# Optimization experiments

Hardware: AMD Instinct MI355X
Metric: run time of the kernel (lower is better)

The kernel has to match this reference:

```python
import jax, jax.numpy as jnp
import numpy as np

COV_LOSS_WT = 1.0


def setup_inputs() -> dict:
    key = jax.random.key(0)
    ks = jax.random.split(key, 6)
    B, T, S, H = 8, 64, 256, 768
    sc = 1.0 / np.sqrt(H)
    return {
        "decoder_outputs": jax.random.normal(ks[0], (B, T, H), jnp.float32),
        "decoder_input_mask": jnp.ones((B, T), jnp.float32),
        "encoder_outputs": jax.random.normal(ks[1], (B, S, H), jnp.float32),
        "enc_padding_mask": jnp.ones((B, S), jnp.float32),
        "coverage": jnp.zeros((B, S), jnp.float32),
        "W_h": (jax.random.normal(ks[2], (H, H), jnp.float32) * sc),
        "W_dec": (jax.random.normal(ks[3], (H, H), jnp.float32) * sc),
        "b_dec": jnp.zeros((H,), jnp.float32),
        "w_c": (jax.random.normal(ks[4], (H,), jnp.float32) * sc),
        "v": (jax.random.normal(ks[5], (H,), jnp.float32) * sc),
    }


def reference(decoder_outputs, decoder_input_mask, encoder_outputs,
              enc_padding_mask, coverage, W_h, W_dec, b_dec, w_c, v):
    # Precompute projections (same math as expanding att_features then adding
    # the coverage feature per step).
    enc_feature = encoder_outputs @ W_h.T                 # [B,S,H]
    dec_fea = decoder_outputs @ W_dec.T + b_dec           # [B,T,H]

    def step(cov, dec_t):
        # cov: [B,S], dec_t: [B,H]
        e = jnp.tanh(enc_feature + dec_t[:, None, :] + cov[:, :, None] * w_c)  # [B,S,H]
        scores = e @ v                                    # [B,S]
        attn = jax.nn.softmax(scores, axis=-1) * enc_padding_mask
        attn = attn / attn.sum(-1, keepdims=True)
        ht = jnp.einsum('bs,bsh->bh', attn, encoder_outputs)
        step_loss = COV_LOSS_WT * jnp.sum(jnp.minimum(attn, cov), axis=-1)     # [B]
        return cov + attn, (ht, attn, step_loss)

    coverage_final, (ht, attn, step_losses) = jax.lax.scan(
        step, coverage, jnp.swapaxes(dec_fea, 0, 1))      # scan over T

    ht_hat = jnp.swapaxes(ht, 0, 1)                       # [B,T,H]
    attn_dist = jnp.swapaxes(attn, 0, 1)                  # [B,T,S]
    converge_loss = jnp.sum(step_losses * decoder_input_mask.T) / jnp.sum(decoder_input_mask)
    return (ht_hat, attn_dist, converge_loss, coverage_final)
```

## Files before the change

kernel.cpp:

```cpp
#include <hip/hip_runtime.h>

#define Bq 8
#define Tq 64
#define Sq 256
#define Hq 768
#define TT 8
#define ST 8

typedef float f32x4 __attribute__((ext_vector_type(4)));
typedef __bf16 bf16x8 __attribute__((ext_vector_type(8)));

#define TANH_SCALE 2.885390081777927f
#define LOG2E 1.4426950408889634f

template <int Ctrl, int Rmask>
__device__ __forceinline__ float dpp_add_f(float v) {
  int t = __builtin_amdgcn_update_dpp(0, __float_as_int(v), Ctrl, Rmask, 0xF, true);
  return v + __int_as_float(t);
}
__device__ __forceinline__ float wave64_sum(float v) {
  v = dpp_add_f<0xB1, 0xF>(v);
  v = dpp_add_f<0x4E, 0xF>(v);
  v = dpp_add_f<0x141, 0xF>(v);
  v = dpp_add_f<0x140, 0xF>(v);
  v = dpp_add_f<0x142, 0xA>(v);
  v = dpp_add_f<0x143, 0xC>(v);
  return __int_as_float(__builtin_amdgcn_readlane(__float_as_int(v), 63));
}

__device__ __forceinline__ uint2 cvt4(f32x4 v) {
  union { __bf16 h[4]; uint2 u; } t;
  t.h[0] = (__bf16)v[0]; t.h[1] = (__bf16)v[1];
  t.h[2] = (__bf16)v[2]; t.h[3] = (__bf16)v[3];
  return t.u;
}

__global__ __launch_bounds__(256, 4) void proj_kernel(
    const float* __restrict__ enc, const float* __restrict__ dec,
    const float* __restrict__ Wh, const float* __restrict__ Wd,
    const float* __restrict__ bd,
    const float* __restrict__ wcvec, const float* __restrict__ vvec,
    __bf16* __restrict__ efh, __bf16* __restrict__ decfh,
    float* __restrict__ w1g, float* __restrict__ lacc,
    unsigned* __restrict__ cnt)
{
  {
    int gidx = blockIdx.x * 256 + threadIdx.x;
    if (gidx < Hq) w1g[gidx] = vvec[gidx] * wcvec[gidx];
    if (gidx < 64) cnt[gidx] = 0u;
    if (gidx == 0) lacc[0] = 0.f;
  }

  __shared__ unsigned short As[2][32][40];
  __shared__ unsigned short Bs[2][64][40];

  int bid = blockIdx.x;
  const float* A; const float* W; bool isEf;
  int bm, bn;
  if (bid < 768) {
    A = enc; W = Wh; isEf = true;
    bm = bid % 64; bn = bid / 64;
  } else {
    bid -= 768;
    A = dec; W = Wd; isEf = false;
    bm = bid % 16; bn = bid / 16;
  }
  const int m0 = bm * 32, n0 = bn * 64;

  const int ti = threadIdx.x;
  const int rowA = ti >> 3, colA = (ti & 7) * 4;
  const int rowB = ti >> 2, colB = (ti & 3) * 8;
  const float* pa = A + (size_t)(m0 + rowA) * Hq + colA;
  const float* pw = W + (size_t)(n0 + rowB) * Hq + colB;

  {
    f32x4 a0 = *(const f32x4*)pa;
    f32x4 w0 = *(const f32x4*)pw, w1 = *(const f32x4*)(pw + 4);
    *(uint2*)&As[0][rowA][colA]     = cvt4(a0);
    *(uint2*)&Bs[0][rowB][colB]     = cvt4(w0);
    *(uint2*)&Bs[0][rowB][colB + 4] = cvt4(w1);
  }
  __syncthreads();

  const int w = ti >> 6, ln = ti & 63;
  const int mh = (w >> 1) * 16, nh = (w & 1) * 32;
  const int rsel = ln & 15, kofe = (ln >> 4) * 8;

  f32x4 acc[2] = {};
  for (int k = 0; k < 24; k++) {
    f32x4 na, nw0, nw1;
    if (k < 23) {
      na  = *(const f32x4*)(pa + (k + 1) * 32);
      nw0 = *(const f32x4*)(pw + (k + 1) * 32);
      nw1 = *(const f32x4*)(pw + (k + 1) * 32 + 4);
    }
    const int cur = k & 1;
    bf16x8 af = *(const bf16x8*)&As[cur][mh + rsel][kofe];
    bf16x8 b0 = *(const bf16x8*)&Bs[cur][nh + rsel][kofe];
    bf16x8 b1 = *(const bf16x8*)&Bs[cur][nh + 16 + rsel][kofe];
    acc[0] = __builtin_amdgcn_mfma_f32_16x16x32_bf16(af, b0, acc[0], 0, 0, 0);
    acc[1] = __builtin_amdgcn_mfma_f32_16x16x32_bf16(af, b1, acc[1], 0, 0, 0);
    if (k < 23) {
      const int nxt = cur ^ 1;
      *(uint2*)&As[nxt][rowA][colA]     = cvt4(na);
      *(uint2*)&Bs[nxt][rowB][colB]     = cvt4(nw0);
      *(uint2*)&Bs[nxt][rowB][colB + 4] = cvt4(nw1);
      __syncthreads();
    }
  }

  const int col = ln & 15, rb = (ln >> 4) * 4;
#pragma unroll
  for (int tn = 0; tn < 2; tn++)
#pragma unroll
    for (int j = 0; j < 4; j++) {
      int r = m0 + mh + rb + j, c = n0 + nh + tn * 16 + col;
      float val = acc[tn][j];
      if (isEf) {
        efh[(size_t)r * Hq + c] =
            (__bf16)__builtin_amdgcn_exp2f(val * TANH_SCALE);
      } else {
        decfh[(size_t)r * Hq + c] =
            (__bf16)__builtin_amdgcn_exp2f((val + bd[c]) * TANH_SCALE);
      }
    }
}

__global__ __launch_bounds__(256, 6) void abscan_kernel(
    const __bf16* __restrict__ efh, const __bf16* __restrict__ decfh,
    const float* __restrict__ vvec, const float* __restrict__ w1g,
    const float* __restrict__ emask, const float* __restrict__ cov0,
    const float* __restrict__ dmask,
    float2* __restrict__ ab,
    float* __restrict__ out_attn, float* __restrict__ out_covf,
    float* __restrict__ lacc, unsigned* __restrict__ cnt)
{
  __shared__ double smem_raw[3280];
  const int bid = blockIdx.x;
  const int tid = threadIdx.x;

  if (bid < 2048) {
    unsigned short (*efs)[772] = (unsigned short(*)[772])smem_raw;
    unsigned short (*dts)[772] = (unsigned short(*)[772])((char*)smem_raw + 12352);
    float (*part)[64][2]       = (float(*)[64][2])((char*)smem_raw + 24704);
    const int kchunk = bid >> 8;
    const int b = (bid >> 5) & 7;
    const int stile = bid & 31;
    const int tt0 = kchunk * TT;
    const int st0 = stile * ST;

    for (int i = tid; i < ST * 192; i += 256) {
      int row = i / 192, c = (i % 192) * 4;
      *(uint2*)&efs[row][c] =
          *(const uint2*)(efh + (size_t)(b * Sq + st0 + row) * Hq + c);
    }
    for (int i = tid; i < TT * 192; i += 256) {
      int row = i / 192, c = (i % 192) * 4;
      *(uint2*)&dts[row][c] =
          *(const uint2*)(decfh + (size_t)(b * Tq + tt0 + row) * Hq + c);
    }
    __syncthreads();

    const int hh = tid >> 6;
    const int pid = tid & 63;
    const int tl = pid >> 3, sl = pid & 7;
    const int hbase = hh * 192;
    const int hbu = __builtin_amdgcn_readfirstlane(hbase);
    const float* vp  = vvec + hbu;
    const float* w1p = w1g + hbu;

    float A = 0.f, B = 0.f;
#define BLO(x) __uint_as_float((x) << 16)
#define BHI(x) __uint_as_float((x) & 0xFFFF0000u)
#pragma unroll 2
    for (int j = 0; j < 192; j += 8) {
      uint2 eu0 = *(const uint2*)&efs[sl][hbase + j];
      uint2 eu1 = *(const uint2*)&efs[sl][hbase + j + 4];
      uint2 du0 = *(const uint2*)&dts[tl][hbase + j];
      uint2 du1 = *(const uint2*)&dts[tl][hbase + j + 4];
      f32x4 v40 = *(const f32x4*)(vp + j);
      f32x4 v41 = *(const f32x4*)(vp + j + 4);
      f32x4 w10 = *(const f32x4*)(w1p + j);
      f32x4 w11 = *(const f32x4*)(w1p + j + 4);
      float e2[8];
      e2[0] = BLO(eu0.x) * BLO(du0.x);
      e2[1] = BHI(eu0.x) * BHI(du0.x);
      e2[2] = BLO(eu0.y) * BLO(du0.y);
      e2[3] = BHI(eu0.y) * BHI(du0.y);
      e2[4] = BLO(eu1.x) * BLO(du1.x);
      e2[5] = BHI(eu1.x) * BHI(du1.x);
      e2[6] = BLO(eu1.y) * BLO(du1.y);
      e2[7] = BHI(eu1.y) * BHI(du1.y);
#pragma unroll
      for (int e = 0; e < 8; e++) {
        float rr = __builtin_amdgcn_rcpf(1.f + e2[e]);
        float t0 = 1.f - 2.f * rr;
        float f1 = 1.f - t0 * t0;
        float vx = (e < 4) ? v40[e] : v41[e - 4];
        float wx = (e < 4) ? w10[e] : w11[e - 4];
        A += vx * t0;
        B += wx * f1;
      }
    }
#undef BLO
#undef BHI

    if (hh != 0) { part[hh - 1][pid][0] = A; part[hh - 1][pid][1] = B; }
    __syncthreads();
    if (hh == 0) {
      union { float2 f; unsigned long long u; } cv;
      cv.f.x = A + part[0][pid][0] + part[1][pid][0] + part[2][pid][0];
      cv.f.y = B + part[0][pid][1] + part[1][pid][1] + part[2][pid][1];
      __hip_atomic_store(
          (unsigned long long*)&ab[(size_t)(b * Tq + tt0 + tl) * Sq + st0 + sl],
          cv.u, __ATOMIC_RELAXED, __HIP_MEMORY_SCOPE_AGENT);
    }
    __syncthreads();
    if (tid == 0)
      __hip_atomic_fetch_add(&cnt[b * 8 + kchunk], 1u,
                             __ATOMIC_RELAXED, __HIP_MEMORY_SCOPE_AGENT);
  } else {
    if (tid >= 64) return;
    const int b = bid - 2048;
    const int ln = tid;
    float dm = dmask[b * Tq + ln];
    float cov[4], em[4], E[4];
    float lp = 0.f;
#pragma unroll
    for (int i = 0; i < 4; i++) {
      cov[i] = cov0[b * Sq + ln + 64 * i];
      em[i]  = emask[b * Sq + ln + 64 * i];
    }
    const unsigned long long* P =
        (const unsigned long long*)(ab + (size_t)b * Tq * Sq + ln);
    union U64 { unsigned long long u; float2 f; };
    U64 cv0[4], cv1[4];

    for (int kc = 0; kc < 8; kc++) {
      unsigned c;
      do {
        c = __hip_atomic_load(&cnt[b * 8 + kc],
                              __ATOMIC_RELAXED, __HIP_MEMORY_SCOPE_AGENT);
      } while (__builtin_amdgcn_readfirstlane(c) < 32u);

      const int tb = kc * 8;
#pragma unroll
      for (int i = 0; i < 4; i++)
        cv0[i].u = __hip_atomic_load(P + (size_t)tb * Sq + 64 * i,
                                     __ATOMIC_RELAXED, __HIP_MEMORY_SCOPE_AGENT);
#pragma unroll
      for (int i = 0; i < 4; i++)
        cv1[i].u = __hip_atomic_load(P + (size_t)(tb + 1) * Sq + 64 * i,
                                     __ATOMIC_RELAXED, __HIP_MEMORY_SCOPE_AGENT);

#pragma unroll
      for (int j = 0; j < 8; j++) {
        const int t = tb + j;
        float s4 = 0.f;
#pragma unroll
        for (int i = 0; i < 4; i++) {
          float sc = cv0[i].f.x + cov[i] * cv0[i].f.y;
          E[i] = __builtin_amdgcn_exp2f(sc * LOG2E) * em[i];
          s4 += E[i];
        }
#pragma unroll
        for (int i = 0; i < 4; i++) {
          cv0[i] = cv1[i];
          if (j < 6)
            cv1[i].u = __hip_atomic_load(P + (size_t)(t + 2) * Sq + 64 * i,
                                         __ATOMIC_RELAXED, __HIP_MEMORY_SCOPE_AGENT);
        }
        float Z = wave64_sum(s4);
        float invZ = __builtin_amdgcn_rcpf(Z);
        float dmt = __shfl(dm, t);
#pragma unroll
        for (int i = 0; i < 4; i++) {
          float at = E[i] * invZ;
          lp += fminf(at, cov[i]) * dmt;
          cov[i] += at;
          out_attn[(size_t)(b * Tq + t) * Sq + ln + 64 * i] = at;
        }
      }
    }

#pragma unroll
    for (int i = 0; i < 4; i++)
      out_covf[b * Sq + ln + 64 * i] = cov[i];
    float wl = wave64_sum(lp);
    if (ln == 0) atomicAdd(lacc, wl);
  }
}

__global__ __launch_bounds__(256) void ht_kernel(
    const float* __restrict__ attn, const float* __restrict__ enc,
    const float* __restrict__ dmask, const float* __restrict__ lacc,
    float* __restrict__ out_ht, float* __restrict__ out_loss)
{
  __shared__ float lat[Sq][8];
  __shared__ float r4[4];
  int bid = blockIdx.x;
  int b = bid / 24, r = bid % 24, tc = r / 3, hc = r % 3;
  int tid = threadIdx.x;
  int h = hc * 256 + tid;
#pragma unroll
  for (int tt = 0; tt < 8; tt++)
    lat[tid][tt] = attn[(size_t)(b * Tq + tc * 8 + tt) * Sq + tid];
  __syncthreads();

  float acc[8] = {};
  const float* ep = enc + (size_t)(b * Sq) * Hq + h;
  for (int sb = 0; sb < Sq; sb += 8) {
    float e[8];
#pragma unroll
    for (int u = 0; u < 8; u++) e[u] = ep[(size_t)(sb + u) * Hq];
#pragma unroll
    for (int u = 0; u < 8; u++) {
      f32x4 a0 = *(const f32x4*)&lat[sb + u][0];
      f32x4 a1 = *(const f32x4*)&lat[sb + u][4];
      acc[0] += a0[0] * e[u]; acc[1] += a0[1] * e[u];
      acc[2] += a0[2] * e[u]; acc[3] += a0[3] * e[u];
      acc[4] += a1[0] * e[u]; acc[5] += a1[1] * e[u];
      acc[6] += a1[2] * e[u]; acc[7] += a1[3] * e[u];
    }
  }
#pragma unroll
  for (int tt = 0; tt < 8; tt++)
    out_ht[(size_t)(b * Tq + tc * 8 + tt) * Hq + h] = acc[tt];

  if (blockIdx.x == 0) {
    float s = 0.f;
    for (int i = tid; i < Bq * Tq; i += 256) s += dmask[i];
#pragma unroll
    for (int off = 32; off; off >>= 1) s += __shfl_xor(s, off);
    int w = tid >> 6, ln = tid & 63;
    if (ln == 0) r4[w] = s;
    __syncthreads();
    if (tid == 0) out_loss[0] = lacc[0] / (r4[0] + r4[1] + r4[2] + r4[3]);
  }
}

extern "C" void kernel_launch(void* const* d_in, const int* in_sizes, int n_in,
                              void* d_out, int out_size, void* d_ws, size_t ws_size,
                              hipStream_t stream) {
  const float* dec   = (const float*)d_in[0];
  const float* dmask = (const float*)d_in[1];
  const float* enc   = (const float*)d_in[2];
  const float* emask = (const float*)d_in[3];
  const float* cov0  = (const float*)d_in[4];
  const float* Wh    = (const float*)d_in[5];
  const float* Wd    = (const float*)d_in[6];
  const float* bd    = (const float*)d_in[7];
  const float* wc    = (const float*)d_in[8];
  const float* vv    = (const float*)d_in[9];
  float* out = (float*)d_out;

  char* ws = (char*)d_ws;
  __bf16*   efh   = (__bf16*)ws;
  __bf16*   decfh = (__bf16*)(ws + 3145728);
  float2*   ab    = (float2*)(ws + 3932160);
  float*    w1g   = (float*)(ws + 4980736);
  float*    lacc  = (float*)(ws + 4983808);
  unsigned* cnt   = (unsigned*)(ws + 4983872);

  const size_t OFF_ATTN = (size_t)Bq * Tq * Hq;
  const size_t OFF_LOSS = OFF_ATTN + (size_t)Bq * Tq * Sq;
  const size_t OFF_COV  = OFF_LOSS + 1;

  proj_kernel<<<960, 256, 0, stream>>>(enc, dec, Wh, Wd, bd, wc, vv,
                                       efh, decfh, w1g, lacc, cnt);
  abscan_kernel<<<2056, 256, 0, stream>>>(efh, decfh, vv, w1g, emask, cov0,
                                          dmask, ab,
                                          out + OFF_ATTN, out + OFF_COV,
                                          lacc, cnt);
  ht_kernel<<<192, 256, 0, stream>>>(out + OFF_ATTN, enc, dmask, lacc,
                                     out, out + OFF_LOSS);
}
```

Measured before the change: 75.33 us.

## Split the attention-score H reduction across two blocks with atomic accumulation

```diff
diff --git a/kernel.cpp b/kernel.cpp
--- a/kernel.cpp
+++ b/kernel.cpp
@@ -42,13 +42,14 @@
     const float* __restrict__ wcvec, const float* __restrict__ vvec,
     __bf16* __restrict__ efh, __bf16* __restrict__ decfh,
     float* __restrict__ w1g, float* __restrict__ lacc,
-    unsigned* __restrict__ cnt)
+    unsigned* __restrict__ cnt, unsigned long long* __restrict__ abz)
 {
   {
     int gidx = blockIdx.x * 256 + threadIdx.x;
     if (gidx < Hq) w1g[gidx] = vvec[gidx] * wcvec[gidx];
     if (gidx < 64) cnt[gidx] = 0u;
     if (gidx == 0) lacc[0] = 0.f;
+    if (gidx < Bq * Tq * Sq) abz[gidx] = 0ULL;
   }
 
   __shared__ unsigned short As[2][32][40];
@@ -126,7 +127,7 @@
     }
 }
 
-__global__ __launch_bounds__(256, 6) void abscan_kernel(
+__global__ __launch_bounds__(256, 8) void abscan_kernel(
     const __bf16* __restrict__ efh, const __bf16* __restrict__ decfh,
     const float* __restrict__ vvec, const float* __restrict__ w1g,
     const float* __restrict__ emask, const float* __restrict__ cov0,
@@ -135,45 +136,47 @@
     float* __restrict__ out_attn, float* __restrict__ out_covf,
     float* __restrict__ lacc, unsigned* __restrict__ cnt)
 {
-  __shared__ double smem_raw[3280];
+  __shared__ double smem_raw[1744];
   const int bid = blockIdx.x;
   const int tid = threadIdx.x;
 
-  if (bid < 2048) {
-    unsigned short (*efs)[772] = (unsigned short(*)[772])smem_raw;
-    unsigned short (*dts)[772] = (unsigned short(*)[772])((char*)smem_raw + 12352);
-    float (*part)[64][2]       = (float(*)[64][2])((char*)smem_raw + 24704);
-    const int kchunk = bid >> 8;
-    const int b = (bid >> 5) & 7;
-    const int stile = bid & 31;
+  if (bid < 4096) {
+    unsigned short (*efs)[388] = (unsigned short(*)[388])smem_raw;
+    unsigned short (*dts)[388] = (unsigned short(*)[388])((char*)smem_raw + 6208);
+    float (*part)[64][2]       = (float(*)[64][2])((char*)smem_raw + 12416);
+    const int kchunk = bid >> 9;
+    const int b = (bid >> 6) & 7;
+    const int stile = (bid >> 1) & 31;
+    const int half = bid & 1;
     const int tt0 = kchunk * TT;
     const int st0 = stile * ST;
-
-    for (int i = tid; i < ST * 192; i += 256) {
-      int row = i / 192, c = (i % 192) * 4;
+    const int hoff = half * 384;
+
+    for (int i = tid; i < ST * 96; i += 256) {
+      int row = i / 96, c = (i % 96) * 4;
       *(uint2*)&efs[row][c] =
-          *(const uint2*)(efh + (size_t)(b * Sq + st0 + row) * Hq + c);
-    }
-    for (int i = tid; i < TT * 192; i += 256) {
-      int row = i / 192, c = (i % 192) * 4;
+          *(const uint2*)(efh + (size_t)(b * Sq + st0 + row) * Hq + hoff + c);
+    }
+    for (int i = tid; i < TT * 96; i += 256) {
+      int row = i / 96, c = (i % 96) * 4;
       *(uint2*)&dts[row][c] =
-          *(const uint2*)(decfh + (size_t)(b * Tq + tt0 + row) * Hq + c);
+          *(const uint2*)(decfh + (size_t)(b * Tq + tt0 + row) * Hq + hoff + c);
     }
     __syncthreads();
 
     const int hh = tid >> 6;
     const int pid = tid & 63;
     const int tl = pid >> 3, sl = pid & 7;
-    const int hbase = hh * 192;
-    const int hbu = __builtin_amdgcn_readfirstlane(hbase);
+    const int hbase = hh * 96;
+    const int hbu = __builtin_amdgcn_readfirstlane(hoff + hbase);
     const float* vp  = vvec + hbu;
     const float* w1p = w1g + hbu;
 
     float A = 0.f, B = 0.f;
 #define BLO(x) __uint_as_float((x) << 16)
-#define BHI(x) __uint_as_float((x) & 0xFFFF0000u)
+#define BHIr(x) __uint_as_float(x)
 #pragma unroll 2
-    for (int j = 0; j < 192; j += 8) {
+    for (int j = 0; j < 96; j += 8) {
       uint2 eu0 = *(const uint2*)&efs[sl][hbase + j];
       uint2 eu1 = *(const uint2*)&efs[sl][hbase + j + 4];
       uint2 du0 = *(const uint2*)&dts[tl][hbase + j];
@@ -184,13 +187,13 @@
       f32x4 w11 = *(const f32x4*)(w1p + j + 4);
       float e2[8];
       e2[0] = BLO(eu0.x) * BLO(du0.x);
-      e2[1] = BHI(eu0.x) * BHI(du0.x);
+      e2[1] = BHIr(eu0.x) * BHIr(du0.x);
       e2[2] = BLO(eu0.y) * BLO(du0.y);
-      e2[3] = BHI(eu0.y) * BHI(du0.y);
+      e2[3] = BHIr(eu0.y) * BHIr(du0.y);
       e2[4] = BLO(eu1.x) * BLO(du1.x);
-      e2[5] = BHI(eu1.x) * BHI(du1.x);
+      e2[5] = BHIr(eu1.x) * BHIr(du1.x);
       e2[6] = BLO(eu1.y) * BLO(du1.y);
-      e2[7] = BHI(eu1.y) * BHI(du1.y);
+      e2[7] = BHIr(eu1.y) * BHIr(du1.y);
 #pragma unroll
       for (int e = 0; e < 8; e++) {
         float rr = __builtin_amdgcn_rcpf(1.f + e2[e]);
@@ -203,17 +206,16 @@
       }
     }
 #undef BLO
-#undef BHI
+#undef BHIr
 
     if (hh != 0) { part[hh - 1][pid][0] = A; part[hh - 1][pid][1] = B; }
     __syncthreads();
     if (hh == 0) {
-      union { float2 f; unsigned long long u; } cv;
-      cv.f.x = A + part[0][pid][0] + part[1][pid][0] + part[2][pid][0];
-      cv.f.y = B + part[0][pid][1] + part[1][pid][1] + part[2][pid][1];
-      __hip_atomic_store(
-          (unsigned long long*)&ab[(size_t)(b * Tq + tt0 + tl) * Sq + st0 + sl],
-          cv.u, __ATOMIC_RELAXED, __HIP_MEMORY_SCOPE_AGENT);
+      float As_ = A + part[0][pid][0] + part[1][pid][0] + part[2][pid][0];
+      float Bs_ = B + part[0][pid][1] + part[1][pid][1] + part[2][pid][1];
+      float2* dst = &ab[(size_t)(b * Tq + tt0 + tl) * Sq + st0 + sl];
+      atomicAdd(&dst->x, As_);
+      atomicAdd(&dst->y, Bs_);
     }
     __syncthreads();
     if (tid == 0)
@@ -221,7 +223,7 @@
                              __ATOMIC_RELAXED, __HIP_MEMORY_SCOPE_AGENT);
   } else {
     if (tid >= 64) return;
-    const int b = bid - 2048;
+    const int b = bid - 4096;
     const int ln = tid;
     float dm = dmask[b * Tq + ln];
     float cov[4], em[4], E[4];
@@ -241,7 +243,7 @@
       do {
         c = __hip_atomic_load(&cnt[b * 8 + kc],
                               __ATOMIC_RELAXED, __HIP_MEMORY_SCOPE_AGENT);
-      } while (__builtin_amdgcn_readfirstlane(c) < 32u);
+      } while (__builtin_amdgcn_readfirstlane(c) < 64u);
 
       const int tb = kc * 8;
 #pragma unroll
@@ -367,8 +369,9 @@
   const size_t OFF_COV  = OFF_LOSS + 1;
 
   proj_kernel<<<960, 256, 0, stream>>>(enc, dec, Wh, Wd, bd, wc, vv,
-                                       efh, decfh, w1g, lacc, cnt);
-  abscan_kernel<<<2056, 256, 0, stream>>>(efh, decfh, vv, w1g, emask, cov0,
+                                       efh, decfh, w1g, lacc, cnt,
+                                       (unsigned long long*)ab);
+  abscan_kernel<<<4104, 256, 0, stream>>>(efh, decfh, vv, w1g, emask, cov0,
                                           dmask, ab,
                                           out + OFF_ATTN, out + OFF_COV,
                                           lacc, cnt);
```

Measured after the change: 80.28 us. 1.07x slower.
